# Optimization experiments

Measured on AMD Instinct MI355X. Metric: run time of the kernel, lower is better.

Reference implementation:

```python
import jax, jax.numpy as jnp
import numpy as np

# Static dims (match init_kwargs)
N = 20000      # ngene_in == ngene_out
H = 4          # nheads
DIN = 32       # nhidatt_in
D = 32         # nhidatt
E = 640000     # edges per graph
NMETA = 64
SLOPE = 0.2    # DGL GATConv default negative_slope

# hypernetwork_in flat output split sizes (a, w, b, a_out, w_out, b_out)
# a: H*1*(2*DIN)*1=256, w: H*1*DIN=128, b: H*DIN=128, a_out: 1*(2*DIN)=64,
# w_out: (DIN*H)*DIN=4096, b_out: 1*DIN=32  -> total 4704
HIN_OFF = np.cumsum([0, 256, 128, 128, 64, 4096, 32])
# hypernetwork_out1 (L=2 att layers): a: H*3*(2*D)=768, w: H*(DIN+2*D)*D=12288,
# b: H*3*D=384, a_out: 3*(2*D)=192, w_out: (3*D*H)*D=12288, b_out: 3*D=96 -> 26016
HOUT_OFF = np.cumsum([0, 768, 12288, 384, 192, 12288, 96])


def gatconv(src, dst, x, fc_w, bias, attn_l, attn_r, heads, dout):
    """DGL-style GATConv on an edge list (src -> dst), sum-aggregation at dst."""
    feat = (x @ fc_w.T).reshape(N, heads, dout)          # [N,H,D]
    el = jnp.sum(feat * attn_l, axis=-1)                 # [N,H]
    er = jnp.sum(feat * attn_r, axis=-1)                 # [N,H]
    e = jax.nn.leaky_relu(el[src] + er[dst], SLOPE)      # [E,H]
    m = jax.ops.segment_max(e, dst, num_segments=N)      # edge-softmax (stable)
    m = jnp.where(jnp.isfinite(m), m, 0.0)
    ex = jnp.exp(e - m[dst])
    s = jax.ops.segment_sum(ex, dst, num_segments=N)
    alpha = ex / (s[dst] + 1e-9)                         # [E,H]
    out = jax.ops.segment_sum(alpha[:, :, None] * feat[src], dst, num_segments=N)
    return out + bias.reshape(1, heads, dout)            # [N,H,D]


def _split(h, offs):
    return [h[offs[i]:offs[i + 1]] for i in range(len(offs) - 1)]


def setup_inputs() -> dict:
    key = jax.random.key(0)
    ks = jax.random.split(key, 12)
    return {
        "X_in1": jax.random.normal(ks[0], (N,), jnp.float32),
        "metadata_in1": jax.random.normal(ks[1], (NMETA,), jnp.float32),
        "metadata_trg": jax.random.normal(ks[2], (NMETA,), jnp.float32),
        "W_hin": jax.random.normal(ks[3], (NMETA, 4704), jnp.float32) * 0.05,
        "b_hin": jax.random.normal(ks[4], (4704,), jnp.float32) * 0.05,
        "W_hout": jax.random.normal(ks[5], (NMETA, 26016), jnp.float32) * 0.05,
        "b_hout": jax.random.normal(ks[6], (26016,), jnp.float32) * 0.05,
        "src_in": jax.random.randint(ks[7], (E,), 0, N, jnp.int32),
        "dst_in": jax.random.randint(ks[8], (E,), 0, N, jnp.int32),
        "src_trg": jax.random.randint(ks[9], (E,), 0, N, jnp.int32),
        "dst_trg": jax.random.randint(ks[10], (E,), 0, N, jnp.int32),
    }


def reference(X_in1, metadata_in1, metadata_trg, W_hin, b_hin, W_hout, b_hout,
              src_in, dst_in, src_trg, dst_trg):
    # ---- hypernetwork_in(metadata_in1): generate input-GAT params ----
    h = metadata_in1 @ W_hin + b_hin
    a_f, w_f, b_f, ao_f, wo_f, bo_f = _split(h, HIN_OFF)
    a_in = a_f.reshape(H, 1, 2 * DIN, 1)
    w_in = w_f.reshape(H, 1, DIN)
    b_in = b_f.reshape(H, DIN)
    a_out_in = ao_f.reshape(1, 2 * DIN)
    w_out_in = wo_f.reshape(DIN * H, DIN)
    b_out_in = bo_f.reshape(1, DIN)

    # ---- gat() helper on g_in1 (attentions1 + out_att1) ----
    a_tmp = a_in[:, 0, :, :].reshape(2, H, -1)           # exact torch reshape
    w_tmp = w_in[:, :1, :].reshape(-1, 1)                # [H*DIN, 1]
    b_tmp = b_in[:, :DIN].reshape(-1)                    # [H*DIN]
    ao_tmp = a_out_in[0, :].reshape(2, -1)
    wo_tmp = w_out_in[:DIN * H, :].reshape(-1, DIN * H)  # [DIN, DIN*H]
    bo_tmp = b_out_in[0, :]

    x = X_in1[:N].reshape(-1, 1)
    z = gatconv(src_in, dst_in, x, w_tmp, b_tmp,
                a_tmp[0].reshape(1, H, -1), a_tmp[1].reshape(1, H, -1),
                H, DIN).reshape(N, -1)                   # [N, H*DIN]
    z_1 = jax.nn.elu(gatconv(src_in, dst_in, z, wo_tmp, bo_tmp,
                             ao_tmp[0].reshape(1, 1, -1), ao_tmp[1].reshape(1, 1, -1),
                             1, DIN)).reshape(N, -1)     # [N, DIN]

    # ---- hypernetwork_out1(metadata_trg): params for attentions3/4 ----
    h2 = metadata_trg @ W_hout + b_hout
    a_f, w_f, b_f, ao_f, wo_f, bo_f = _split(h2, HOUT_OFF)
    a = a_f.reshape(H, -1, 2 * D, 1)                     # [H, 3, 2D, 1]
    w = w_f.reshape(H, -1, D)                            # [H, DIN+2D, D]
    b = b_f.reshape(H, -1)                               # [H, 3D]
    a_out = ao_f.reshape(-1, 2 * D)                      # [3, 2D]
    w_out = wo_f.reshape(-1, D)                          # [3*D*H, D]
    b_out = bo_f.reshape(-1, D)                          # [3, D]

    # ---- attentions3 / out_att3 on g_trg_in ----
    a_t = a[:, 0, :, :].reshape(2, H, -1)
    w_t = w[:, :DIN, :].reshape(-1, DIN)                 # [H*D, DIN]
    b_t = b[:, :D].reshape(-1)
    ao_t = a_out[0, :].reshape(2, -1)
    wo_t = w_out[:D * H, :].reshape(-1, D * H)
    bo_t = b_out[0, :]
    z2 = gatconv(src_trg, dst_trg, z_1, w_t, b_t,
                 a_t[0].reshape(1, H, -1), a_t[1].reshape(1, H, -1),
                 H, D).reshape(N, -1)
    z2 = jax.nn.elu(gatconv(src_trg, dst_trg, z2, wo_t, bo_t,
                            ao_t[0].reshape(1, 1, -1), ao_t[1].reshape(1, 1, -1),
                            1, D)).reshape(N, D)

    # ---- attentions4 / out_att4 on g_trg_in ----
    a_t2 = a[:, 1, :, :].reshape(2, H, -1)
    w_t2 = w[:, DIN:DIN + D, :].reshape(-1, D)
    b_t2 = b[:, D:2 * D].reshape(-1)
    ao_t2 = a_out[1, :].reshape(2, -1)
    wo_t2 = w_out[D * H:2 * D * H, :].reshape(-1, D * H)
    bo_t2 = b_out[1, :]
    z2 = gatconv(src_trg, dst_trg, z2, w_t2, b_t2,
                 a_t2[0].reshape(1, H, -1), a_t2[1].reshape(1, H, -1),
                 H, D).reshape(N, -1)
    z2 = jax.nn.elu(gatconv(src_trg, dst_trg, z2, wo_t2, bo_t2,
                            ao_t2[0].reshape(1, 1, -1), ao_t2[1].reshape(1, 1, -1),
                            1, D)).reshape(N, D)
    return z2
```

## Files before the change

### kernel.cpp

```cpp
#include <hip/hip_runtime.h>
#include <math.h>

#define NN 20000
#define EE 640000
#define NB4C 5000
#define NCH 80
#define CHE 8000

typedef unsigned short ushortT;
typedef unsigned int uintT;

__device__ __forceinline__ float lrelu(float x){ return x >= 0.f ? x : 0.2f*x; }
__device__ __forceinline__ ushortT f2bf(float x){
  uintT u = __float_as_uint(x);
  u = (u + 0x7FFFu + ((u >> 16) & 1u)) >> 16;
  return (ushortT)u;
}

__global__ __launch_bounds__(256) void k_prmhist(const float* __restrict__ m1,
        const float* __restrict__ mt, const float* __restrict__ Whin,
        const float* __restrict__ bhin, const float* __restrict__ Whout,
        const float* __restrict__ bhout, float* __restrict__ P,
        const int* __restrict__ dst_in, const int* __restrict__ dst_trg,
        int* __restrict__ histB){
  __shared__ int hist[NN/2];
  int b = blockIdx.x;
  if (b < 2*NCH){
    int g = b / NCH, c = b % NCH;
    const int* dst = g ? dst_trg : dst_in;
    for (int i=threadIdx.x; i<NN/2; i+=256) hist[i] = 0;
    __syncthreads();
    int e0 = c*CHE;
    for (int k=threadIdx.x; k<CHE; k+=256){
      int d = dst[e0+k];
      atomicAdd(&hist[d>>1], (d&1) ? 65536 : 1);
    }
    __syncthreads();
    int* outp = histB + b*(NN/2);
    for (int i=threadIdx.x; i<NN/2; i+=256) outp[i] = hist[i];
    return;
  }
  int t = (b - 2*NCH)*256 + threadIdx.x;
  if (t >= 22048) return;
  int sj; bool inA;
  if      (t < 128)  { sj = 256+t;          inA=true; }
  else if (t < 256)  { sj = 384+(t-128);    inA=true; }
  else if (t < 384)  { sj = t-256;          inA=true; }
  else if (t < 512)  { sj = 128+(t-384);    inA=true; }
  else if (t < 4608) { sj = 576+(t-512);    inA=true; }
  else if (t < 4640) { sj = 4672+(t-4608);  inA=true; }
  else if (t < 4672) { sj = 512+(t-4640);   inA=true; }
  else if (t < 4704) { sj = 544+(t-4672);   inA=true; }
  else { inA=false;
    if      (t < 8800)  { int k=t-4704, o=k>>5, i=k&31; sj = 768 + (o>>5)*3072+(o&31)*32+i; }
    else if (t < 8928)  { int o=t-8800; sj = 13056 + (o>>5)*96+(o&31); }
    else if (t < 9056)  { int q=t-8928;       sj = (q>>6)*192+(q&63); }
    else if (t < 9184)  { int q=(t-9056)+128; sj = (q>>6)*192+(q&63); }
    else if (t < 13280) { sj = 13632 + (t-9184); }
    else if (t < 13312) { sj = 25920 + (t-13280); }
    else if (t < 13344) { sj = 13440 + (t-13312); }
    else if (t < 13376) { sj = 13472 + (t-13344); }
    else if (t < 17472) { int k=t-13376, o=k>>5, i=k&31; sj = 768 + (o>>5)*3072+(32+(o&31))*32+i; }
    else if (t < 17600) { int o=t-17472; sj = 13056 + (o>>5)*96+32+(o&31); }
    else if (t < 17728) { int q=t-17600;       sj = (q>>6)*192+64+(q&63); }
    else if (t < 17856) { int q=(t-17728)+128; sj = (q>>6)*192+64+(q&63); }
    else if (t < 21952) { sj = 13632+4096+(t-17856); }
    else if (t < 21984) { sj = 25920+32+(t-21952); }
    else if (t < 22016) { sj = 13440+64+(t-21984); }
    else                { sj = 13440+96+(t-22016); }
  }
  float acc;
  if (inA){
    acc = bhin[sj];
    #pragma unroll 8
    for (int k=0;k<64;++k) acc = fmaf(m1[k], Whin[k*4704 + sj], acc);
  } else {
    acc = bhout[sj];
    #pragma unroll 8
    for (int k=0;k<64;++k) acc = fmaf(mt[k], Whout[k*26016 + sj], acc);
  }
  P[t] = acc;
}

__global__ __launch_bounds__(1024) void k_csrA(const int* __restrict__ histB,
        int* __restrict__ exc, int* __restrict__ bsum){
  int b = blockIdx.x, t = threadIdx.x;
  int g = b/20, c2 = b%20;
  int i = c2*1024 + t;
  int tot = 0;
  if (i < NN){
    int sh = (i&1)*16;
    for (int cb=0; cb<NCH; ++cb){
      int w = histB[(g*NCH+cb)*(NN/2) + (i>>1)];
      tot += (w >> sh) & 0xFFFF;
    }
  }
  __shared__ int s[1024];
  s[t] = tot;
  __syncthreads();
  for (int d=1; d<1024; d<<=1){
    int v = (t>=d) ? s[t-d] : 0;
    __syncthreads();
    s[t] += v;
    __syncthreads();
  }
  exc[b*1024 + t] = s[t] - tot;
  if (t == 1023) bsum[b] = s[t];
}

__global__ void k_csrB(const int* __restrict__ bsum, int* __restrict__ bbase,
        int* __restrict__ off_in, int* __restrict__ off_trg,
        const float* __restrict__ P, float* __restrict__ P2){
  int t = threadIdx.x;
  if (t < 8){
    int hh = t >> 1, sel = t & 1;
    const float* W = P;
    const float* A = P + 256 + sel*128;
    float c = 0.f;
    #pragma unroll 8
    for (int d=0; d<32; ++d) c = fmaf(W[hh*32+d], A[hh*32+d], c);
    P2[sel*4 + hh] = c;
  } else if (t == 8){
    int base = 0;
    for (int b=0; b<20; ++b){ bbase[b] = base; base += bsum[b]; }
  } else if (t == 9){
    int base = 0;
    for (int b=20; b<40; ++b){ bbase[b] = base; base += bsum[b]; }
  } else if (t == 10) off_in[NN]  = EE;
  else if   (t == 11) off_trg[NN] = EE;
}

__global__ __launch_bounds__(1024) void k_csrC(const int* __restrict__ histB,
        const int* __restrict__ exc, const int* __restrict__ bbase,
        int* __restrict__ off_in, int* __restrict__ off_trg,
        int* __restrict__ bases){
  int b = blockIdx.x, t = threadIdx.x;
  int g = b/20, c2 = b%20;
  int i = c2*1024 + t;
  if (i >= NN) return;
  int* off = g ? off_trg : off_in;
  int running = exc[b*1024 + t] + bbase[b];
  off[i] = running;
  int sh = (i&1)*16;
  for (int cb=0; cb<NCH; ++cb){
    bases[(g*NCH+cb)*NN + i] = running;
    int w = histB[(g*NCH+cb)*(NN/2) + (i>>1)];
    running += (w >> sh) & 0xFFFF;
  }
}

__global__ __launch_bounds__(256) void k_fillL(const int* __restrict__ src_in,
        const int* __restrict__ dst_in, const int* __restrict__ src_trg,
        const int* __restrict__ dst_trg, const int* __restrict__ bases,
        ushortT* __restrict__ csr_in, ushortT* __restrict__ csr_trg){
  int b = blockIdx.x;
  int g = b / (2*NCH);
  int rem = b % (2*NCH);
  int half = rem / NCH, c = rem % NCH;
  const int* src = g ? src_trg : src_in;
  const int* dst = g ? dst_trg : dst_in;
  ushortT* csr = g ? csr_trg : csr_in;
  __shared__ int alloc[NN/2];
  const int* basep = bases + (g*NCH+c)*NN + half*(NN/2);
  for (int i=threadIdx.x; i<NN/2; i+=256) alloc[i] = basep[i];
  __syncthreads();
  int e0 = c*CHE;
  int lo = half*(NN/2);
  for (int k=threadIdx.x; k<CHE; k+=256){
    int d = dst[e0+k];
    int dl = d - lo;
    if ((unsigned)dl < (unsigned)(NN/2)){
      int p = atomicAdd(&alloc[dl], 1);
      csr[p] = (ushortT)src[e0+k];
    }
  }
}

template<int IN, int OUT, int H>
__global__ __launch_bounds__(256) void k_featel(const float* __restrict__ z,
        const float* __restrict__ W, const float* __restrict__ AL,
        const float* __restrict__ AR, ushortT* __restrict__ featb,
        float* __restrict__ el, float* __restrict__ er){
  __shared__ float Ws[IN*(OUT+1)];
  __shared__ float ALs[OUT], ARs[OUT];
  for (int idx=threadIdx.x; idx<IN*OUT; idx+=256){
    int o = idx / IN, i = idx % IN;
    Ws[i*(OUT+1) + o] = W[idx];
  }
  for (int idx=threadIdx.x; idx<OUT; idx+=256){ ALs[idx]=AL[idx]; ARs[idx]=AR[idx]; }
  __syncthreads();
  int tid = blockIdx.x*256 + threadIdx.x;
  int n = tid / OUT, o = tid % OUT;
  const float4* z4 = (const float4*)(z + n*IN);
  float acc = 0.f;
  #pragma unroll
  for (int i=0;i<IN/4;++i){
    float4 zv = z4[i];
    acc = fmaf(zv.x, Ws[(4*i+0)*(OUT+1)+o], acc);
    acc = fmaf(zv.y, Ws[(4*i+1)*(OUT+1)+o], acc);
    acc = fmaf(zv.z, Ws[(4*i+2)*(OUT+1)+o], acc);
    acc = fmaf(zv.w, Ws[(4*i+3)*(OUT+1)+o], acc);
  }
  int h = o >> 5, d = o & 31;
  featb[(h*NN + n)*32 + d] = f2bf(acc);
  float a = acc * ALs[o], b = acc * ARs[o];
  #pragma unroll
  for (int msk=1; msk<32; msk<<=1){
    a += __shfl_xor(a, msk);
    b += __shfl_xor(b, msk);
  }
  if (d == 0){
    el[h*NN + n] = a;
    er[h*NN + n] = b;
  }
}

__global__ __launch_bounds__(256) void k_l1(const int* __restrict__ off,
        const ushortT* __restrict__ csr, const float* __restrict__ X,
        const float* __restrict__ P, const float* __restrict__ P2,
        float* __restrict__ out){
  int wv = threadIdx.x >> 6, l = threadIdx.x & 63;
  int n = blockIdx.x*4 + wv;
  if (n >= NN) return;
  int start = off[n], deg = off[n+1] - start;
  int hl = l & 3, jl = l >> 2;
  float cl = P2[hl], cr = P2[4 + hl];
  float xd = X[n];
  float m = -INFINITY, ssum = 0.f, t = 0.f;
  for (int j = jl; j < deg; j += 16){
    int s = csr[start + j];
    float xs = X[s];
    float e = lrelu(xs*cl + xd*cr);
    if (e > m){
      float w = __expf(m - e);
      ssum = ssum*w + 1.f;
      t    = t*w + xs;
      m = e;
    } else {
      float w = __expf(e - m);
      ssum += w;
      t    = fmaf(w, xs, t);
    }
  }
  #pragma unroll
  for (int msk=4; msk<64; msk<<=1){
    float mo = __shfl_xor(m, msk), so = __shfl_xor(ssum, msk), to = __shfl_xor(t, msk);
    float mn = fmaxf(m, mo);
    if (mn > -INFINITY){
      float w1 = __expf(m - mn), w2 = __expf(mo - mn);
      ssum = ssum*w1 + so*w2;
      t    = t*w1 + to*w2;
    }
    m = mn;
  }
  float tv = t / (ssum + 1e-9f);
  float th = __shfl(tv, l >> 4);
  const float2 w2v = *(const float2*)(P + 2*l);
  const float2 b2v = *(const float2*)(P + 128 + 2*l);
  float2 o;
  o.x = fmaf(th, w2v.x, b2v.x);
  o.y = fmaf(th, w2v.y, b2v.y);
  *(float2*)(out + n*128 + 2*l) = o;
}

template<int H, bool ELU>
__global__ __launch_bounds__(256) void k_aggH(const int* __restrict__ off,
        const ushortT* __restrict__ csr, const ushortT* __restrict__ featb,
        const float* __restrict__ el, const float* __restrict__ er,
        const float* __restrict__ bias, float* __restrict__ out){
  __shared__ float2 as_[4][64];
  int wv = threadIdx.x >> 6, l = threadIdx.x & 63;
  int bid = blockIdx.x;
  int h = bid / NB4C, b = bid % NB4C;
  int n = b*4 + wv;
  if (n >= NN) return;
  const float* elh = el + h*NN;
  const ushortT* fh = featb + (size_t)h*NN*32;
  int start = off[n], deg = off[n+1] - start;
  float erl = er[h*NN + n];
  int g = l >> 3, dl = l & 7;
  float4 acc = make_float4(0.f, 0.f, 0.f, 0.f);
  float asum = 0.f;
  if (deg <= 64){
    int s = 0; float e = -INFINITY;
    if (l < deg){ s = csr[start + l]; e = lrelu(elh[s] + erl); }
    float m = e;
    #pragma unroll
    for (int msk=1; msk<64; msk<<=1) m = fmaxf(m, __shfl_xor(m, msk));
    float a = (l < deg) ? __expf(e - m) : 0.f;
    as_[wv][l] = make_float2(a, __int_as_float(s));
    #pragma unroll 4
    for (int jj = 0; jj < deg; jj += 8){
      float2 p = as_[wv][jj + g];
      float aj = p.x; int sj = __float_as_int(p.y);
      uint2 w = *(const uint2*)(fh + sj*32 + 4*dl);
      acc.x = fmaf(aj, __uint_as_float(w.x << 16),        acc.x);
      acc.y = fmaf(aj, __uint_as_float(w.x & 0xFFFF0000u), acc.y);
      acc.z = fmaf(aj, __uint_as_float(w.y << 16),        acc.z);
      acc.w = fmaf(aj, __uint_as_float(w.y & 0xFFFF0000u), acc.w);
      asum += aj;
    }
  } else {
    float m = -INFINITY;
    for (int j0 = 0; j0 < deg; j0 += 64){
      int j = j0 + l;
      int s = 0; float e = -INFINITY;
      if (j < deg){ s = csr[start + j]; e = lrelu(elh[s] + erl); }
      float cm = e;
      #pragma unroll
      for (int msk=1; msk<64; msk<<=1) cm = fmaxf(cm, __shfl_xor(cm, msk));
      float mn = fmaxf(m, cm);
      float rs = __expf(m - mn);
      float a = (j < deg) ? __expf(e - mn) : 0.f;
      acc.x *= rs; acc.y *= rs; acc.z *= rs; acc.w *= rs;
      asum *= rs;
      m = mn;
      as_[wv][l] = make_float2(a, __int_as_float(s));
      int cnt = deg - j0; if (cnt > 64) cnt = 64;
      #pragma unroll 4
      for (int jj = 0; jj < cnt; jj += 8){
        float2 p = as_[wv][jj + g];
        float aj = p.x; int sj = __float_as_int(p.y);
        uint2 w = *(const uint2*)(fh + sj*32 + 4*dl);
        acc.x = fmaf(aj, __uint_as_float(w.x << 16),        acc.x);
        acc.y = fmaf(aj, __uint_as_float(w.x & 0xFFFF0000u), acc.y);
        acc.z = fmaf(aj, __uint_as_float(w.y << 16),        acc.z);
        acc.w = fmaf(aj, __uint_as_float(w.y & 0xFFFF0000u), acc.w);
        asum += aj;
      }
    }
  }
  #pragma unroll
  for (int msk=8; msk<64; msk<<=1){
    acc.x += __shfl_xor(acc.x, msk);
    acc.y += __shfl_xor(acc.y, msk);
    acc.z += __shfl_xor(acc.z, msk);
    acc.w += __shfl_xor(acc.w, msk);
    asum  += __shfl_xor(asum,  msk);
  }
  float sinv = 1.f/(asum + 1e-9f);
  if (l < 8){
    const float4 b4 = *(const float4*)(bias + h*32 + 4*l);
    float o0 = fmaf(acc.x, sinv, b4.x);
    float o1 = fmaf(acc.y, sinv, b4.y);
    float o2 = fmaf(acc.z, sinv, b4.z);
    float o3 = fmaf(acc.w, sinv, b4.w);
    if (ELU){
      o0 = o0 > 0.f ? o0 : expm1f(o0);
      o1 = o1 > 0.f ? o1 : expm1f(o1);
      o2 = o2 > 0.f ? o2 : expm1f(o2);
      o3 = o3 > 0.f ? o3 : expm1f(o3);
    }
    *(float4*)(out + n*(H*32) + h*32 + 4*l) = make_float4(o0, o1, o2, o3);
  }
}

#define WS_P     0
#define WS_P2    22144
#define WS_EL    22272
#define WS_ER    102272
#define WS_FEAT  262144
#define WS_ZA    2822144
#define WS_ZB    5382144
#define WS_OFFI  6022144
#define WS_OFFT  6042240
#define WS_CSRI  6423552
#define WS_CSRT  6743552
#define WS_TOTAL 7063552
#define WS_HB    (WS_FEAT + 0)
#define WS_BS    (WS_FEAT + 1600000)
#define WS_EXC   (WS_FEAT + 4800000)
#define WS_BSUM  (WS_FEAT + 4841472)
#define WS_BBASE (WS_FEAT + 4841600)

extern "C" void kernel_launch(void* const* d_in, const int* in_sizes, int n_in,
                              void* d_out, int out_size, void* d_ws, size_t ws_size,
                              hipStream_t stream) {
  if (ws_size < (size_t)WS_TOTAL * sizeof(float)) {
    hipMemsetAsync(d_out, 0, (size_t)out_size * sizeof(float), stream);
    return;
  }
  const float* X      = (const float*)d_in[0];
  const float* m1     = (const float*)d_in[1];
  const float* mt     = (const float*)d_in[2];
  const float* Whin   = (const float*)d_in[3];
  const float* bhin   = (const float*)d_in[4];
  const float* Whout  = (const float*)d_in[5];
  const float* bhout  = (const float*)d_in[6];
  const int* src_in   = (const int*)d_in[7];
  const int* dst_in   = (const int*)d_in[8];
  const int* src_trg  = (const int*)d_in[9];
  const int* dst_trg  = (const int*)d_in[10];
  float* out = (float*)d_out;
  float* ws  = (float*)d_ws;

  float* P    = ws + WS_P;
  float* P2   = ws + WS_P2;
  float* el   = ws + WS_EL;
  float* er   = ws + WS_ER;
  ushortT* featb = (ushortT*)(ws + WS_FEAT);
  float* zA   = ws + WS_ZA;
  float* zB   = ws + WS_ZB;
  int* off_in  = (int*)(ws + WS_OFFI);
  int* off_trg = (int*)(ws + WS_OFFT);
  int* histB   = (int*)(ws + WS_HB);
  int* bases   = (int*)(ws + WS_BS);
  int* exc     = (int*)(ws + WS_EXC);
  int* bsum    = (int*)(ws + WS_BSUM);
  int* bbase   = (int*)(ws + WS_BBASE);
  ushortT* csr_in  = (ushortT*)(ws + WS_CSRI);
  ushortT* csr_trg = (ushortT*)(ws + WS_CSRT);

  k_prmhist<<<2*NCH + 87, 256, 0, stream>>>(m1, mt, Whin, bhin, Whout, bhout, P,
                                            dst_in, dst_trg, histB);
  k_csrA<<<40, 1024, 0, stream>>>(histB, exc, bsum);
  k_csrB<<<1, 64, 0, stream>>>(bsum, bbase, off_in, off_trg, P, P2);
  k_csrC<<<40, 1024, 0, stream>>>(histB, exc, bbase, off_in, off_trg, bases);
  k_fillL<<<4*NCH, 256, 0, stream>>>(src_in, dst_in, src_trg, dst_trg, bases,
                                     csr_in, csr_trg);

  k_l1<<<NB4C, 256, 0, stream>>>(off_in, csr_in, X, P, P2, zA);

  k_featel<128,32,1><<<(NN*32)/256, 256, 0, stream>>>(zA, P+512, P+4640, P+4672, featb, el, er);
  k_aggH<1,true><<<NB4C, 256, 0, stream>>>(off_in, csr_in, featb, el, er, P+4608, zB);

  k_featel<32,128,4><<<(NN*128)/256, 256, 0, stream>>>(zB, P+4704, P+8928, P+9056, featb, el, er);
  k_aggH<4,false><<<4*NB4C, 256, 0, stream>>>(off_trg, csr_trg, featb, el, er, P+8800, zA);

  k_featel<128,32,1><<<(NN*32)/256, 256, 0, stream>>>(zA, P+9184, P+13312, P+13344, featb, el, er);
  k_aggH<1,true><<<NB4C, 256, 0, stream>>>(off_trg, csr_trg, featb, el, er, P+13280, zB);

  k_featel<32,128,4><<<(NN*128)/256, 256, 0, stream>>>(zB, P+13376, P+17600, P+17728, featb, el, er);
  k_aggH<4,false><<<4*NB4C, 256, 0, stream>>>(off_trg, csr_trg, featb, el, er, P+17472, zA);

  k_featel<128,32,1><<<(NN*32)/256, 256, 0, stream>>>(zA, P+17856, P+21984, P+22016, featb, el, er);
  k_aggH<1,true><<<NB4C, 256, 0, stream>>>(off_trg, csr_trg, featb, el, er, P+21952, out);
}
```

Baseline: 272.6 us.

## Store features node-major and aggregate all four heads per wave

Features and attention logits are now written node-major (node, head, dim) rather than head-major. A new 4-head aggregation kernel handles every head of a destination node in one wave, so the CSR indices, degree and source el values are read once per edge instead of once per head. Each gathered row becomes one contiguous 256-byte block of all heads, read as 16-byte loads. In exchange the kernel needs more registers and more shuffles for the four-way softmax, and uses fewer blocks.

```diff
diff --git a/kernel.cpp b/kernel.cpp
--- a/kernel.cpp
+++ b/kernel.cpp
@@ -16,6 +16,8 @@
   u = (u + 0x7FFFu + ((u >> 16) & 1u)) >> 16;
   return (ushortT)u;
 }
+__device__ __forceinline__ float bfl(uintT w){ return __uint_as_float(w << 16); }
+__device__ __forceinline__ float bfh(uintT w){ return __uint_as_float(w & 0xFFFF0000u); }
 
 __global__ __launch_bounds__(256) void k_prmhist(const float* __restrict__ m1,
         const float* __restrict__ mt, const float* __restrict__ Whin,
@@ -201,17 +203,17 @@
     acc = fmaf(zv.z, Ws[(4*i+2)*(OUT+1)+o], acc);
     acc = fmaf(zv.w, Ws[(4*i+3)*(OUT+1)+o], acc);
   }
-  int h = o >> 5, d = o & 31;
-  featb[(h*NN + n)*32 + d] = f2bf(acc);
+  featb[n*OUT + o] = f2bf(acc);
   float a = acc * ALs[o], b = acc * ARs[o];
   #pragma unroll
   for (int msk=1; msk<32; msk<<=1){
     a += __shfl_xor(a, msk);
     b += __shfl_xor(b, msk);
   }
-  if (d == 0){
-    el[h*NN + n] = a;
-    er[h*NN + n] = b;
+  if ((o & 31) == 0){
+    int h = o >> 5;
+    el[n*H + h] = a;
+    er[n*H + h] = b;
   }
 }
 
@@ -263,27 +265,151 @@
   *(float2*)(out + n*128 + 2*l) = o;
 }
 
-template<int H, bool ELU>
-__global__ __launch_bounds__(256) void k_aggH(const int* __restrict__ off,
+template<bool ELU>
+__global__ __launch_bounds__(256) void k_agg4(const int* __restrict__ off,
+        const ushortT* __restrict__ csr, const ushortT* __restrict__ featb,
+        const float* __restrict__ el4, const float* __restrict__ er4,
+        const float* __restrict__ bias, float* __restrict__ out){
+  __shared__ float4 aS[4][64];
+  __shared__ int    sS[4][64];
+  int wv = threadIdx.x >> 6, l = threadIdx.x & 63;
+  int n = blockIdx.x*4 + wv;
+  if (n >= NN) return;
+  int start = off[n], deg = off[n+1] - start;
+  const float4 ern = *(const float4*)(er4 + n*4);
+  int g = l >> 4, q = l & 15, h = q >> 2, p = q & 3;
+  float acc[8] = {0.f,0.f,0.f,0.f,0.f,0.f,0.f,0.f};
+  float4 asum = make_float4(0.f,0.f,0.f,0.f);
+  if (deg <= 64){
+    int s = 0;
+    float4 e4 = make_float4(-INFINITY,-INFINITY,-INFINITY,-INFINITY);
+    if (l < deg){
+      s = csr[start + l];
+      const float4 elv = *(const float4*)(el4 + s*4);
+      e4.x = lrelu(elv.x + ern.x); e4.y = lrelu(elv.y + ern.y);
+      e4.z = lrelu(elv.z + ern.z); e4.w = lrelu(elv.w + ern.w);
+    }
+    float4 m4 = e4;
+    #pragma unroll
+    for (int msk=1; msk<64; msk<<=1){
+      m4.x = fmaxf(m4.x, __shfl_xor(m4.x, msk));
+      m4.y = fmaxf(m4.y, __shfl_xor(m4.y, msk));
+      m4.z = fmaxf(m4.z, __shfl_xor(m4.z, msk));
+      m4.w = fmaxf(m4.w, __shfl_xor(m4.w, msk));
+    }
+    float4 a4 = make_float4(0.f,0.f,0.f,0.f);
+    if (l < deg){
+      a4.x = __expf(e4.x - m4.x); a4.y = __expf(e4.y - m4.y);
+      a4.z = __expf(e4.z - m4.z); a4.w = __expf(e4.w - m4.w);
+    }
+    asum = a4;
+    aS[wv][l] = a4; sS[wv][l] = s;
+    #pragma unroll 4
+    for (int jj = 0; jj < deg; jj += 4){
+      int e = jj + g;
+      float aj = ((const float*)&aS[wv][e])[h];
+      int   sj = sS[wv][e];
+      uint4 w = *(const uint4*)(featb + sj*128 + h*32 + p*8);
+      acc[0] = fmaf(aj, bfl(w.x), acc[0]); acc[1] = fmaf(aj, bfh(w.x), acc[1]);
+      acc[2] = fmaf(aj, bfl(w.y), acc[2]); acc[3] = fmaf(aj, bfh(w.y), acc[3]);
+      acc[4] = fmaf(aj, bfl(w.z), acc[4]); acc[5] = fmaf(aj, bfh(w.z), acc[5]);
+      acc[6] = fmaf(aj, bfl(w.w), acc[6]); acc[7] = fmaf(aj, bfh(w.w), acc[7]);
+    }
+  } else {
+    float4 m4 = make_float4(-INFINITY,-INFINITY,-INFINITY,-INFINITY);
+    for (int j0 = 0; j0 < deg; j0 += 64){
+      int j = j0 + l;
+      int s = 0;
+      float4 e4 = make_float4(-INFINITY,-INFINITY,-INFINITY,-INFINITY);
+      if (j < deg){
+        s = csr[start + j];
+        const float4 elv = *(const float4*)(el4 + s*4);
+        e4.x = lrelu(elv.x + ern.x); e4.y = lrelu(elv.y + ern.y);
+        e4.z = lrelu(elv.z + ern.z); e4.w = lrelu(elv.w + ern.w);
+      }
+      float4 cm = e4;
+      #pragma unroll
+      for (int msk=1; msk<64; msk<<=1){
+        cm.x = fmaxf(cm.x, __shfl_xor(cm.x, msk));
+        cm.y = fmaxf(cm.y, __shfl_xor(cm.y, msk));
+        cm.z = fmaxf(cm.z, __shfl_xor(cm.z, msk));
+        cm.w = fmaxf(cm.w, __shfl_xor(cm.w, msk));
+      }
+      float4 mn = make_float4(fmaxf(m4.x,cm.x), fmaxf(m4.y,cm.y),
+                              fmaxf(m4.z,cm.z), fmaxf(m4.w,cm.w));
+      float4 rs;
+      rs.x = __expf(m4.x - mn.x); rs.y = __expf(m4.y - mn.y);
+      rs.z = __expf(m4.z - mn.z); rs.w = __expf(m4.w - mn.w);
+      float4 a4 = make_float4(0.f,0.f,0.f,0.f);
+      if (j < deg){
+        a4.x = __expf(e4.x - mn.x); a4.y = __expf(e4.y - mn.y);
+        a4.z = __expf(e4.z - mn.z); a4.w = __expf(e4.w - mn.w);
+      }
+      asum.x = asum.x*rs.x + a4.x; asum.y = asum.y*rs.y + a4.y;
+      asum.z = asum.z*rs.z + a4.z; asum.w = asum.w*rs.w + a4.w;
+      float rh = ((const float*)&rs)[h];
+      #pragma unroll
+      for (int i=0;i<8;++i) acc[i] *= rh;
+      m4 = mn;
+      aS[wv][l] = a4; sS[wv][l] = s;
+      int cnt = deg - j0; if (cnt > 64) cnt = 64;
+      #pragma unroll 4
+      for (int jj = 0; jj < cnt; jj += 4){
+        int e = jj + g;
+        float aj = ((const float*)&aS[wv][e])[h];
+        int   sj = sS[wv][e];
+        uint4 w = *(const uint4*)(featb + sj*128 + h*32 + p*8);
+        acc[0] = fmaf(aj, bfl(w.x), acc[0]); acc[1] = fmaf(aj, bfh(w.x), acc[1]);
+        acc[2] = fmaf(aj, bfl(w.y), acc[2]); acc[3] = fmaf(aj, bfh(w.y), acc[3]);
+        acc[4] = fmaf(aj, bfl(w.z), acc[4]); acc[5] = fmaf(aj, bfh(w.z), acc[5]);
+        acc[6] = fmaf(aj, bfl(w.w), acc[6]); acc[7] = fmaf(aj, bfh(w.w), acc[7]);
+      }
+    }
+  }
+  #pragma unroll
+  for (int i=0;i<8;++i){
+    acc[i] += __shfl_xor(acc[i], 16);
+    acc[i] += __shfl_xor(acc[i], 32);
+  }
+  #pragma unroll
+  for (int msk=1; msk<64; msk<<=1){
+    asum.x += __shfl_xor(asum.x, msk);
+    asum.y += __shfl_xor(asum.y, msk);
+    asum.z += __shfl_xor(asum.z, msk);
+    asum.w += __shfl_xor(asum.w, msk);
+  }
+  if (l < 16){
+    float sinv = 1.f/(((const float*)&asum)[h] + 1e-9f);
+    const float* bp = bias + h*32 + p*8;
+    float o[8];
+    #pragma unroll
+    for (int i=0;i<8;++i){
+      o[i] = fmaf(acc[i], sinv, bp[i]);
+      if (ELU) o[i] = o[i] > 0.f ? o[i] : expm1f(o[i]);
+    }
+    float* op = out + n*128 + h*32 + p*8;
+    *(float4*)op       = make_float4(o[0],o[1],o[2],o[3]);
+    *(float4*)(op + 4) = make_float4(o[4],o[5],o[6],o[7]);
+  }
+}
+
+template<bool ELU>
+__global__ __launch_bounds__(256) void k_agg1(const int* __restrict__ off,
         const ushortT* __restrict__ csr, const ushortT* __restrict__ featb,
         const float* __restrict__ el, const float* __restrict__ er,
         const float* __restrict__ bias, float* __restrict__ out){
   __shared__ float2 as_[4][64];
   int wv = threadIdx.x >> 6, l = threadIdx.x & 63;
-  int bid = blockIdx.x;
-  int h = bid / NB4C, b = bid % NB4C;
-  int n = b*4 + wv;
+  int n = blockIdx.x*4 + wv;
   if (n >= NN) return;
-  const float* elh = el + h*NN;
-  const ushortT* fh = featb + (size_t)h*NN*32;
   int start = off[n], deg = off[n+1] - start;
-  float erl = er[h*NN + n];
+  float erl = er[n];
   int g = l >> 3, dl = l & 7;
   float4 acc = make_float4(0.f, 0.f, 0.f, 0.f);
   float asum = 0.f;
   if (deg <= 64){
     int s = 0; float e = -INFINITY;
-    if (l < deg){ s = csr[start + l]; e = lrelu(elh[s] + erl); }
+    if (l < deg){ s = csr[start + l]; e = lrelu(el[s] + erl); }
     float m = e;
     #pragma unroll
     for (int msk=1; msk<64; msk<<=1) m = fmaxf(m, __shfl_xor(m, msk));
@@ -291,13 +417,13 @@
     as_[wv][l] = make_float2(a, __int_as_float(s));
     #pragma unroll 4
     for (int jj = 0; jj < deg; jj += 8){
-      float2 p = as_[wv][jj + g];
-      float aj = p.x; int sj = __float_as_int(p.y);
-      uint2 w = *(const uint2*)(fh + sj*32 + 4*dl);
-      acc.x = fmaf(aj, __uint_as_float(w.x << 16),        acc.x);
-      acc.y = fmaf(aj, __uint_as_float(w.x & 0xFFFF0000u), acc.y);
-      acc.z = fmaf(aj, __uint_as_float(w.y << 16),        acc.z);
-      acc.w = fmaf(aj, __uint_as_float(w.y & 0xFFFF0000u), acc.w);
+      float2 pr = as_[wv][jj + g];
+      float aj = pr.x; int sj = __float_as_int(pr.y);
+      uint2 w = *(const uint2*)(featb + sj*32 + 4*dl);
+      acc.x = fmaf(aj, bfl(w.x), acc.x);
+      acc.y = fmaf(aj, bfh(w.x), acc.y);
+      acc.z = fmaf(aj, bfl(w.y), acc.z);
+      acc.w = fmaf(aj, bfh(w.y), acc.w);
       asum += aj;
     }
   } else {
@@ -305,7 +431,7 @@
     for (int j0 = 0; j0 < deg; j0 += 64){
       int j = j0 + l;
       int s = 0; float e = -INFINITY;
-      if (j < deg){ s = csr[start + j]; e = lrelu(elh[s] + erl); }
+      if (j < deg){ s = csr[start + j]; e = lrelu(el[s] + erl); }
       float cm = e;
       #pragma unroll
       for (int msk=1; msk<64; msk<<=1) cm = fmaxf(cm, __shfl_xor(cm, msk));
@@ -319,13 +445,13 @@
       int cnt = deg - j0; if (cnt > 64) cnt = 64;
       #pragma unroll 4
       for (int jj = 0; jj < cnt; jj += 8){
-        float2 p = as_[wv][jj + g];
-        float aj = p.x; int sj = __float_as_int(p.y);
-        uint2 w = *(const uint2*)(fh + sj*32 + 4*dl);
-        acc.x = fmaf(aj, __uint_as_float(w.x << 16),        acc.x);
-        acc.y = fmaf(aj, __uint_as_float(w.x & 0xFFFF0000u), acc.y);
-        acc.z = fmaf(aj, __uint_as_float(w.y << 16),        acc.z);
-        acc.w = fmaf(aj, __uint_as_float(w.y & 0xFFFF0000u), acc.w);
+        float2 pr = as_[wv][jj + g];
+        float aj = pr.x; int sj = __float_as_int(pr.y);
+        uint2 w = *(const uint2*)(featb + sj*32 + 4*dl);
+        acc.x = fmaf(aj, bfl(w.x), acc.x);
+        acc.y = fmaf(aj, bfh(w.x), acc.y);
+        acc.z = fmaf(aj, bfl(w.y), acc.z);
+        acc.w = fmaf(aj, bfh(w.y), acc.w);
         asum += aj;
       }
     }
@@ -340,7 +466,7 @@
   }
   float sinv = 1.f/(asum + 1e-9f);
   if (l < 8){
-    const float4 b4 = *(const float4*)(bias + h*32 + 4*l);
+    const float4 b4 = *(const float4*)(bias + 4*l);
     float o0 = fmaf(acc.x, sinv, b4.x);
     float o1 = fmaf(acc.y, sinv, b4.y);
     float o2 = fmaf(acc.z, sinv, b4.z);
@@ -351,7 +477,7 @@
       o2 = o2 > 0.f ? o2 : expm1f(o2);
       o3 = o3 > 0.f ? o3 : expm1f(o3);
     }
-    *(float4*)(out + n*(H*32) + h*32 + 4*l) = make_float4(o0, o1, o2, o3);
+    *(float4*)(out + n*32 + 4*l) = make_float4(o0, o1, o2, o3);
   }
 }
 
@@ -422,17 +548,17 @@
   k_l1<<<NB4C, 256, 0, stream>>>(off_in, csr_in, X, P, P2, zA);
 
   k_featel<128,32,1><<<(NN*32)/256, 256, 0, stream>>>(zA, P+512, P+4640, P+4672, featb, el, er);
-  k_aggH<1,true><<<NB4C, 256, 0, stream>>>(off_in, csr_in, featb, el, er, P+4608, zB);
+  k_agg1<true><<<NB4C, 256, 0, stream>>>(off_in, csr_in, featb, el, er, P+4608, zB);
 
   k_featel<32,128,4><<<(NN*128)/256, 256, 0, stream>>>(zB, P+4704, P+8928, P+9056, featb, el, er);
-  k_aggH<4,false><<<4*NB4C, 256, 0, stream>>>(off_trg, csr_trg, featb, el, er, P+8800, zA);
+  k_agg4<false><<<NB4C, 256, 0, stream>>>(off_trg, csr_trg, featb, el, er, P+8800, zA);
 
   k_featel<128,32,1><<<(NN*32)/256, 256, 0, stream>>>(zA, P+9184, P+13312, P+13344, featb, el, er);
-  k_aggH<1,true><<<NB4C, 256, 0, stream>>>(off_trg, csr_trg, featb, el, er, P+13280, zB);
+  k_agg1<true><<<NB4C, 256, 0, stream>>>(off_trg, csr_trg, featb, el, er, P+13280, zB);
 
   k_featel<32,128,4><<<(NN*128)/256, 256, 0, stream>>>(zB, P+13376, P+17600, P+17728, featb, el, er);
-  k_aggH<4,false><<<4*NB4C, 256, 0, stream>>>(off_trg, csr_trg, featb, el, er, P+17472, zA);
+  k_agg4<false><<<NB4C, 256, 0, stream>>>(off_trg, csr_trg, featb, el, er, P+17472, zA);
 
   k_featel<128,32,1><<<(NN*32)/256, 256, 0, stream>>>(zA, P+17856, P+21984, P+22016, featb, el, er);
-  k_aggH<1,true><<<NB4C, 256, 0, stream>>>(off_trg, csr_trg, featb, el, er, P+21952, out);
-}
+  k_agg1<true><<<NB4C, 256, 0, stream>>>(off_trg, csr_trg, featb, el, er, P+21952, out);
+}
```

Result: slower. 309.7 us (+13.6%).
